# Kernel optimization log

Hardware: AMD Instinct MI355X
Metric: run time of the kernel (lower is better)

Reference implementation:

```python
import jax, jax.numpy as jnp
import numpy as np

DIM = 512
MOVE_EMBED_DIM = 64
NUM_BUCKETS = 64
EMBED = 768
B = 8192
STEPS = 10


def setup_inputs() -> dict:
    key = jax.random.key(0)
    ks = jax.random.split(key, 16)
    def g(i, shape, scale=0.02):
        return jax.random.normal(ks[i], shape, jnp.float32) * scale
    return {
        "boards": jax.random.normal(ks[0], (STEPS, B, EMBED), jnp.float32),
        "flags": jax.random.randint(ks[1], (STEPS - 2, B), 0, 2).astype(bool),
        "themes": jax.random.randint(ks[2], (B,), 0, 10),
        "moves": jax.random.randint(ks[3], (B,), 0, NUM_BUCKETS),
        "start": jax.random.uniform(ks[4], (DIM,), jnp.float32),
        "red_w": g(5, (DIM, EMBED)), "red_b": jnp.zeros((DIM,), jnp.float32),
        "ca_w": g(6, (DIM, DIM)), "ca_b": jnp.zeros((DIM,), jnp.float32),
        "cb_w": g(7, (DIM, DIM)), "cb_b": jnp.zeros((DIM,), jnp.float32),
        "move_emb": g(8, (NUM_BUCKETS, MOVE_EMBED_DIM), 1.0),
        "fc1_w": g(9, (DIM, DIM + MOVE_EMBED_DIM)), "fc1_b": jnp.zeros((DIM,), jnp.float32),
        "fc2_w": g(10, (DIM, DIM)), "fc2_b": jnp.zeros((DIM,), jnp.float32),
        "fc3_w": g(11, (1024, DIM)), "fc3_b": jnp.zeros((1024,), jnp.float32),
        "fc4_w": g(12, (1024, 1024)), "fc4_b": jnp.zeros((1024,), jnp.float32),
        "fc5_w": g(13, (512, 1024)), "fc5_b": jnp.zeros((512,), jnp.float32),
        "out_w": g(14, (1, 512)), "out_b": jnp.zeros((1,), jnp.float32),
    }


def reference(boards, flags, themes, moves, start, red_w, red_b, ca_w, ca_b,
              cb_w, cb_b, move_emb, fc1_w, fc1_b, fc2_w, fc2_b, fc3_w, fc3_b,
              fc4_w, fc4_b, fc5_w, fc5_b, out_w, out_b):
    bsz = boards.shape[1]
    # boards[0:2] are never masked; boards[2:10] are zeroed where flags are False
    full_flags = jnp.concatenate([jnp.ones((2, bsz), bool), flags], axis=0)  # [10,B]
    emb = jnp.where(full_flags[:, :, None], boards, 0.0)                     # [10,B,E]
    # shared dim reducer + relu applied to all 10 positions at once
    e = jax.nn.relu(jnp.einsum('sbe,de->sbd', emb, red_w) + red_b)           # [10,B,DIM]
    # precompute combiner_b contribution for every step (batched GEMM)
    eb = jnp.einsum('sbd,kd->sbk', e, cb_w) + cb_b                           # [10,B,DIM]
    # combiner_a(start)+combiner_b(e0) == combiner_a(h0)+... with h0 = start broadcast
    h0 = jnp.broadcast_to(start, (bsz, DIM))
    def step(h, eb_t):
        return jnp.tanh(h @ ca_w.T + ca_b + eb_t), None
    h, _ = jax.lax.scan(step, h0, eb)                                        # [B,DIM]
    # dropout layers are identity in eval mode
    m = move_emb[moves]                                                      # [B,MOVE_EMBED_DIM]
    x = jax.nn.relu(jnp.concatenate([h, m], axis=-1) @ fc1_w.T + fc1_b)
    x = jax.nn.relu(x @ fc2_w.T + fc2_b)
    x = jax.nn.relu(x @ fc3_w.T + fc3_b)
    x = jax.nn.relu(x @ fc4_w.T + fc4_b)
    x = jax.nn.relu(x @ fc5_w.T + fc5_b)
    return x @ out_w.T + out_b                                               # [B,1]
```

## Files before the change

### kernel.cpp

```cpp
#include <hip/hip_runtime.h>
#include <math.h>

#define BATCH  8192
#define EMBED  768
#define DIMD   512
#define MEDIM  64
#define NSTEP  10

typedef __bf16 bf16x8 __attribute__((ext_vector_type(8)));
typedef float  f32x4  __attribute__((ext_vector_type(4)));

__device__ __forceinline__ void load16_lds(const void* g, void* l)
{
    auto* gp = (__attribute__((address_space(1))) char*)(uintptr_t)g;
    auto* lp = (__attribute__((address_space(3))) char*)(unsigned int)(uintptr_t)l;
    __builtin_amdgcn_global_load_lds(gp, lp, 16, 0, 0);
}

#define BN 128
#define BK 32

template<int ACT, bool ADDEB, bool GATHER, int BMT>
__global__ __launch_bounds__(256)
void gemm_bf16(const __bf16* __restrict__ A, const __bf16* __restrict__ Bt,
               const float* __restrict__ bias, const __bf16* __restrict__ add,
               const __bf16* __restrict__ me, const int* __restrict__ moves,
               __bf16* __restrict__ C, int M, int N, int K)
{
    constexpr int NG = (BMT + BN) / 16;
    constexpr int AG = BMT / 16;
    constexpr int MR = BMT / 32;

    __shared__ __bf16 lds[(BMT + BN) * BK];

    const int nwg  = gridDim.x * gridDim.y;
    const int orig = blockIdx.y * gridDim.x + blockIdx.x;
    const int cpx  = nwg >> 3;
    const int swz  = (orig & 7) * cpx + (orig >> 3);
    const int bx   = swz % gridDim.x;
    const int by   = swz / gridDim.x;

    const int tid  = threadIdx.x;
    const int wave = tid >> 6;
    const int lane = tid & 63;
    const int row0 = by * BMT;
    const int col0 = bx * BN;

    const int wr = (wave >> 1) * (BMT / 2);
    const int wc = (wave & 1) * 64;
    const int fr = lane & 15;
    const int fk = (lane >> 4) * 8;

    const int srow = lane >> 2;
    const int skk  = (lane & 3) * 8;

    f32x4 acc[MR][4] = {};

    for (int k0 = 0; k0 < K; k0 += BK) {
#pragma unroll
        for (int ci = 0; ci < NG / 4; ++ci) {
            const int c = ci * 4 + wave;
            const int r = c * 16 + srow;
            const __bf16* g;
            if (c < AG) {
                if (GATHER) {
                    const int grow = row0 + r;
                    g = (k0 < DIMD)
                        ? (A  + (size_t)grow * DIMD + k0 + skk)
                        : (me + (size_t)moves[grow] * MEDIM + (k0 - DIMD) + skk);
                } else {
                    g = A + (size_t)(row0 + r) * K + k0 + skk;
                }
            } else {
                g = Bt + (size_t)(col0 + (r - BMT)) * K + k0 + skk;
            }
            load16_lds(g, &lds[c * 512]);
        }
        __syncthreads();

        const __bf16* As = lds;
        const __bf16* Bs = lds + BMT * BK;
        bf16x8 af[MR], bfr[4];
#pragma unroll
        for (int m = 0; m < MR; ++m)
            af[m] = *(const bf16x8*)&As[(wr + m * 16 + fr) * BK + fk];
#pragma unroll
        for (int n = 0; n < 4; ++n)
            bfr[n] = *(const bf16x8*)&Bs[(wc + n * 16 + fr) * BK + fk];
#pragma unroll
        for (int m = 0; m < MR; ++m)
#pragma unroll
            for (int n = 0; n < 4; ++n)
                acc[m][n] = __builtin_amdgcn_mfma_f32_16x16x32_bf16(
                                af[m], bfr[n], acc[m][n], 0, 0, 0);
        __syncthreads();
    }

#pragma unroll
    for (int m = 0; m < MR; ++m) {
#pragma unroll
        for (int n = 0; n < 4; ++n) {
            const int cc = col0 + wc + n * 16 + fr;
            const float bb = bias[cc];
#pragma unroll
            for (int j = 0; j < 4; ++j) {
                const int rr = row0 + wr + m * 16 + (lane >> 4) * 4 + j;
                float v = acc[m][n][j] + bb;
                if (ADDEB) v += (float)add[(size_t)rr * N + cc];
                if (ACT == 1) v = fmaxf(v, 0.0f);
                if (ACT == 2) {
                    const float p = __expf(2.0f * v);
                    v = 1.0f - 2.0f / (p + 1.0f);
                }
                C[(size_t)rr * N + cc] = (__bf16)v;
            }
        }
    }
}

__global__ __launch_bounds__(256)
void gemm_red_f32A(const float* __restrict__ A, const __bf16* __restrict__ Bt,
                   const float* __restrict__ bias, const int* __restrict__ flags,
                   __bf16* __restrict__ C, int M, int N, int K)
{
    __shared__ float  Af[128 * 32];
    __shared__ __bf16 Bs[128 * 32];

    const int nwg  = gridDim.x * gridDim.y;
    const int orig = blockIdx.y * gridDim.x + blockIdx.x;
    const int cpx  = nwg >> 3;
    const int swz  = (orig & 7) * cpx + (orig >> 3);
    const int bx   = swz % gridDim.x;
    const int by   = swz / gridDim.x;

    const int tid  = threadIdx.x;
    const int wave = tid >> 6;
    const int lane = tid & 63;
    const int row0 = by * 128;
    const int col0 = bx * BN;

    const int wr = (wave >> 1) * 64;
    const int wc = (wave & 1) * 64;
    const int fr = lane & 15;
    const int fk = (lane >> 4) * 8;

    const int asrow = lane >> 3;
    const int akc   = (lane & 7) ^ asrow;
    const int bsrow = lane >> 2;
    const int bskk  = (lane & 3) * 8;

    f32x4 acc[4][4] = {};

    for (int k0 = 0; k0 < K; k0 += BK) {
#pragma unroll
        for (int ci = 0; ci < 6; ++ci) {
            const int c = ci * 4 + wave;
            if (c < 16) {
                const float* g = A + (size_t)(row0 + c * 8 + asrow) * K + k0 + akc * 4;
                load16_lds(g, (char*)Af + c * 1024);
            } else {
                const int cb = c - 16;
                const __bf16* g = Bt + (size_t)(col0 + cb * 16 + bsrow) * K + k0 + bskk;
                load16_lds(g, (char*)Bs + cb * 1024);
            }
        }
        __syncthreads();

        bf16x8 af[4], bfr[4];
#pragma unroll
        for (int m = 0; m < 4; ++m) {
            const int r = wr + m * 16 + fr;
            const int kc0 = fk >> 2;
            const f32x4 v0 = *(const f32x4*)&Af[r * 32 + ((kc0    ) ^ (r & 7)) * 4];
            const f32x4 v1 = *(const f32x4*)&Af[r * 32 + ((kc0 + 1) ^ (r & 7)) * 4];
#pragma unroll
            for (int j = 0; j < 4; ++j) {
                af[m][j]     = (__bf16)v0[j];
                af[m][j + 4] = (__bf16)v1[j];
            }
        }
#pragma unroll
        for (int n = 0; n < 4; ++n)
            bfr[n] = *(const bf16x8*)&Bs[(wc + n * 16 + fr) * BK + fk];
#pragma unroll
        for (int m = 0; m < 4; ++m)
#pragma unroll
            for (int n = 0; n < 4; ++n)
                acc[m][n] = __builtin_amdgcn_mfma_f32_16x16x32_bf16(
                                af[m], bfr[n], acc[m][n], 0, 0, 0);
        __syncthreads();
    }

    float fl[4][4];
#pragma unroll
    for (int m = 0; m < 4; ++m)
#pragma unroll
        for (int j = 0; j < 4; ++j) {
            const int rr = row0 + wr + m * 16 + (lane >> 4) * 4 + j;
            const int s = rr >> 13, b = rr & 8191;
            fl[m][j] = (s < 2) ? 1.0f
                               : (flags[(size_t)(s - 2) * BATCH + b] ? 1.0f : 0.0f);
        }

#pragma unroll
    for (int m = 0; m < 4; ++m) {
#pragma unroll
        for (int n = 0; n < 4; ++n) {
            const int cc = col0 + wc + n * 16 + fr;
            const float bb = bias[cc];
#pragma unroll
            for (int j = 0; j < 4; ++j) {
                const int rr = row0 + wr + m * 16 + (lane >> 4) * 4 + j;
                const float a = (fl[m][j] != 0.0f) ? (acc[m][n][j] + bb) : bb;
                C[(size_t)rr * N + cc] = (__bf16)fmaxf(a, 0.0f);
            }
        }
    }
}

enum : int { W_RED = 0, W_CA = 393216, W_CB = 655360, W_FC1 = 917504,
             W_FC2 = 1212416, W_FC3 = 1474560, W_FC4 = 1998848,
             W_FC5 = 3047424, W_ME = 3571712, W_TOTAL = 3575808 };

__global__ __launch_bounds__(256)
void cvt_weights(const float* __restrict__ w0, const float* __restrict__ w1,
                 const float* __restrict__ w2, const float* __restrict__ w3,
                 const float* __restrict__ w4, const float* __restrict__ w5,
                 const float* __restrict__ w6, const float* __restrict__ w7,
                 const float* __restrict__ w8, __bf16* __restrict__ dst)
{
    const int idx = blockIdx.x * 256 + threadIdx.x;
    if (idx >= W_TOTAL / 8) return;
    const int e = idx * 8;
    const float* src; int off;
    if      (e < W_CA)  { src = w0; off = W_RED; }
    else if (e < W_CB)  { src = w1; off = W_CA; }
    else if (e < W_FC1) { src = w2; off = W_CB; }
    else if (e < W_FC2) { src = w3; off = W_FC1; }
    else if (e < W_FC3) { src = w4; off = W_FC2; }
    else if (e < W_FC4) { src = w5; off = W_FC3; }
    else if (e < W_FC5) { src = w6; off = W_FC4; }
    else if (e < W_ME)  { src = w7; off = W_FC5; }
    else                { src = w8; off = W_ME; }
    const float4 v0 = ((const float4*)(src + (e - off)))[0];
    const float4 v1 = ((const float4*)(src + (e - off)))[1];
    bf16x8 o;
    o[0] = (__bf16)v0.x; o[1] = (__bf16)v0.y; o[2] = (__bf16)v0.z; o[3] = (__bf16)v0.w;
    o[4] = (__bf16)v1.x; o[5] = (__bf16)v1.y; o[6] = (__bf16)v1.z; o[7] = (__bf16)v1.w;
    *(bf16x8*)(dst + (size_t)e) = o;
}

__global__ __launch_bounds__(256)
void gemv_start(const float* __restrict__ caw, const float* __restrict__ cab,
                const float* __restrict__ start, float* __restrict__ tmp)
{
    __shared__ float s[DIMD];
    for (int i = threadIdx.x; i < DIMD; i += 256) s[i] = start[i];
    __syncthreads();
    const int n = blockIdx.x * 256 + threadIdx.x;
    const float4* w = (const float4*)(caw + (size_t)n * DIMD);
    float acc = 0.0f;
#pragma unroll 8
    for (int k = 0; k < DIMD / 4; ++k) {
        const float4 wv = w[k];
        acc += wv.x * s[k * 4] + wv.y * s[k * 4 + 1] +
               wv.z * s[k * 4 + 2] + wv.w * s[k * 4 + 3];
    }
    tmp[n] = acc + cab[n];
}

__global__ __launch_bounds__(256)
void h1_init(const float* __restrict__ tmp, const __bf16* __restrict__ eb0,
             __bf16* __restrict__ h)
{
    const int idx = blockIdx.x * 256 + threadIdx.x;
    const int c8 = idx & 63;
    const bf16x8 e = ((const bf16x8*)eb0)[idx];
    bf16x8 o;
#pragma unroll
    for (int j = 0; j < 8; ++j) {
        const float v = tmp[c8 * 8 + j] + (float)e[j];
        const float p = __expf(2.0f * v);
        o[j] = (__bf16)(1.0f - 2.0f / (p + 1.0f));
    }
    ((bf16x8*)h)[idx] = o;
}

__global__ __launch_bounds__(256)
void out_head(const __bf16* __restrict__ x, const float* __restrict__ out_w,
              const float* __restrict__ out_b, float* __restrict__ out)
{
    const int wid  = threadIdx.x >> 6;
    const int lane = threadIdx.x & 63;
    const int row  = blockIdx.x * 4 + wid;
    const bf16x8 xv = *(const bf16x8*)(x + (size_t)row * DIMD + lane * 8);
    const float4 w0 = ((const float4*)out_w)[lane * 2];
    const float4 w1 = ((const float4*)out_w)[lane * 2 + 1];
    float s = (float)xv[0] * w0.x + (float)xv[1] * w0.y + (float)xv[2] * w0.z +
              (float)xv[3] * w0.w + (float)xv[4] * w1.x + (float)xv[5] * w1.y +
              (float)xv[6] * w1.z + (float)xv[7] * w1.w;
#pragma unroll
    for (int off = 32; off; off >>= 1) s += __shfl_down(s, off, 64);
    if (lane == 0) out[row] = s + out_b[0];
}

extern "C" void kernel_launch(void* const* d_in, const int* in_sizes, int n_in,
                              void* d_out, int out_size, void* d_ws, size_t ws_size,
                              hipStream_t stream)
{
    const float* boards  = (const float*)d_in[0];
    const int*   flags   = (const int*)  d_in[1];
    const int*   moves   = (const int*)  d_in[3];
    const float* start   = (const float*)d_in[4];
    const float* red_w   = (const float*)d_in[5];
    const float* red_b   = (const float*)d_in[6];
    const float* ca_w    = (const float*)d_in[7];
    const float* ca_b    = (const float*)d_in[8];
    const float* cb_w    = (const float*)d_in[9];
    const float* cb_b    = (const float*)d_in[10];
    const float* move_emb= (const float*)d_in[11];
    const float* fc1_w   = (const float*)d_in[12];
    const float* fc1_b   = (const float*)d_in[13];
    const float* fc2_w   = (const float*)d_in[14];
    const float* fc2_b   = (const float*)d_in[15];
    const float* fc3_w   = (const float*)d_in[16];
    const float* fc3_b   = (const float*)d_in[17];
    const float* fc4_w   = (const float*)d_in[18];
    const float* fc4_b   = (const float*)d_in[19];
    const float* fc5_w   = (const float*)d_in[20];
    const float* fc5_b   = (const float*)d_in[21];
    const float* out_w   = (const float*)d_in[22];
    const float* out_b   = (const float*)d_in[23];

    __bf16* wsb = (__bf16*)d_ws;
    __bf16* wpool  = wsb;
    __bf16* e_all  = wsb + 3575808;
    __bf16* eb_all = wsb + 45518848;
    __bf16* hA     = wsb + 87461888;
    __bf16* hB     = wsb + 91656192;
    float*  tmpv   = (float*)(wsb + 95850496);
    __bf16* x1     = wsb + 96874496;
    __bf16* x2     = wsb + 101068800;
    __bf16* x3     = wsb + 105263104;
    __bf16* x4     = wsb + 113651712;
    __bf16* x5     = wsb + 122040320;

    const dim3 blk(256);

    cvt_weights<<<1746, blk, 0, stream>>>(red_w, ca_w, cb_w, fc1_w, fc2_w,
                                          fc3_w, fc4_w, fc5_w, move_emb, wpool);
    gemv_start<<<2, blk, 0, stream>>>(ca_w, ca_b, start, tmpv);

    gemm_red_f32A<<<dim3(4, 640), blk, 0, stream>>>(
        boards, wpool + W_RED, red_b, flags, e_all, NSTEP * BATCH, DIMD, EMBED);
    gemm_bf16<0, false, false, 128><<<dim3(4, 640), blk, 0, stream>>>(
        e_all, wpool + W_CB, cb_b, nullptr, nullptr, nullptr, eb_all,
        NSTEP * BATCH, DIMD, DIMD);

    h1_init<<<2048, blk, 0, stream>>>(tmpv, eb_all, hA);

    __bf16* hcur = hA;
    __bf16* hnxt = hB;
    for (int s = 1; s < NSTEP; ++s) {
        const __bf16* ebs = eb_all + (size_t)s * BATCH * DIMD;
        gemm_bf16<2, true, false, 64><<<dim3(4, 128), blk, 0, stream>>>(
            hcur, wpool + W_CA, ca_b, ebs, nullptr, nullptr, hnxt,
            BATCH, DIMD, DIMD);
        __bf16* t = hcur; hcur = hnxt; hnxt = t;
    }

    gemm_bf16<1, false, true, 128><<<dim3(4, 64), blk, 0, stream>>>(
        hcur, wpool + W_FC1, fc1_b, nullptr, wpool + W_ME, moves, x1,
        BATCH, DIMD, DIMD + MEDIM);
    gemm_bf16<1, false, false, 128><<<dim3(4, 64), blk, 0, stream>>>(
        x1, wpool + W_FC2, fc2_b, nullptr, nullptr, nullptr, x2, BATCH, DIMD, DIMD);
    gemm_bf16<1, false, false, 128><<<dim3(8, 64), blk, 0, stream>>>(
        x2, wpool + W_FC3, fc3_b, nullptr, nullptr, nullptr, x3, BATCH, 1024, DIMD);
    gemm_bf16<1, false, false, 128><<<dim3(8, 64), blk, 0, stream>>>(
        x3, wpool + W_FC4, fc4_b, nullptr, nullptr, nullptr, x4, BATCH, 1024, 1024);
    gemm_bf16<1, false, false, 128><<<dim3(4, 64), blk, 0, stream>>>(
        x4, wpool + W_FC5, fc5_b, nullptr, nullptr, nullptr, x5, BATCH, DIMD, 1024);

    out_head<<<BATCH / 4, blk, 0, stream>>>(x5, out_w, out_b, (float*)d_out);
}
```

Before: 491.8 us.

## Double-buffer LDS tiles in GEMM kernels to overlap loads with MFMA

Result: faster. 452.8 us (-7.9%).

```diff
diff --git a/kernel.cpp b/kernel.cpp
--- a/kernel.cpp
+++ b/kernel.cpp
@@ -31,7 +31,7 @@
     constexpr int AG = BMT / 16;
     constexpr int MR = BMT / 32;
 
-    __shared__ __bf16 lds[(BMT + BN) * BK];
+    __shared__ __bf16 lds[2][(BMT + BN) * BK];
 
     const int nwg  = gridDim.x * gridDim.y;
     const int orig = blockIdx.y * gridDim.x + blockIdx.x;
@@ -54,9 +54,7 @@
     const int srow = lane >> 2;
     const int skk  = (lane & 3) * 8;
 
-    f32x4 acc[MR][4] = {};
-
-    for (int k0 = 0; k0 < K; k0 += BK) {
+    auto stage = [&](int buf, int k0) {
 #pragma unroll
         for (int ci = 0; ci < NG / 4; ++ci) {
             const int c = ci * 4 + wave;
@@ -74,12 +72,22 @@
             } else {
                 g = Bt + (size_t)(col0 + (r - BMT)) * K + k0 + skk;
             }
-            load16_lds(g, &lds[c * 512]);
-        }
-        __syncthreads();
-
-        const __bf16* As = lds;
-        const __bf16* Bs = lds + BMT * BK;
+            load16_lds(g, &lds[buf][c * 512]);
+        }
+    };
+
+    f32x4 acc[MR][4] = {};
+
+    stage(0, 0);
+    __syncthreads();
+
+    const int NT = K / BK;
+    int cur = 0;
+    for (int t = 0; t < NT; ++t) {
+        if (t + 1 < NT) stage(cur ^ 1, (t + 1) * BK);
+
+        const __bf16* As = lds[cur];
+        const __bf16* Bs = lds[cur] + BMT * BK;
         bf16x8 af[MR], bfr[4];
 #pragma unroll
         for (int m = 0; m < MR; ++m)
@@ -94,6 +102,7 @@
                 acc[m][n] = __builtin_amdgcn_mfma_f32_16x16x32_bf16(
                                 af[m], bfr[n], acc[m][n], 0, 0, 0);
         __syncthreads();
+        cur ^= 1;
     }
 
 #pragma unroll
@@ -123,8 +132,8 @@
                    const float* __restrict__ bias, const int* __restrict__ flags,
                    __bf16* __restrict__ C, int M, int N, int K)
 {
-    __shared__ float  Af[128 * 32];
-    __shared__ __bf16 Bs[128 * 32];
+    __shared__ float  Af[2][128 * 32];
+    __shared__ __bf16 Bs[2][128 * 32];
 
     const int nwg  = gridDim.x * gridDim.y;
     const int orig = blockIdx.y * gridDim.x + blockIdx.x;
@@ -149,30 +158,38 @@
     const int bsrow = lane >> 2;
     const int bskk  = (lane & 3) * 8;
 
-    f32x4 acc[4][4] = {};
-
-    for (int k0 = 0; k0 < K; k0 += BK) {
+    auto stage = [&](int buf, int k0) {
 #pragma unroll
         for (int ci = 0; ci < 6; ++ci) {
             const int c = ci * 4 + wave;
             if (c < 16) {
                 const float* g = A + (size_t)(row0 + c * 8 + asrow) * K + k0 + akc * 4;
-                load16_lds(g, (char*)Af + c * 1024);
+                load16_lds(g, (char*)Af[buf] + c * 1024);
             } else {
                 const int cb = c - 16;
                 const __bf16* g = Bt + (size_t)(col0 + cb * 16 + bsrow) * K + k0 + bskk;
-                load16_lds(g, (char*)Bs + cb * 1024);
+                load16_lds(g, (char*)Bs[buf] + cb * 1024);
             }
         }
-        __syncthreads();
+    };
+
+    f32x4 acc[4][4] = {};
+
+    stage(0, 0);
+    __syncthreads();
+
+    const int NT = K / BK;
+    int cur = 0;
+    for (int t = 0; t < NT; ++t) {
+        if (t + 1 < NT) stage(cur ^ 1, (t + 1) * BK);
 
         bf16x8 af[4], bfr[4];
 #pragma unroll
         for (int m = 0; m < 4; ++m) {
             const int r = wr + m * 16 + fr;
             const int kc0 = fk >> 2;
-            const f32x4 v0 = *(const f32x4*)&Af[r * 32 + ((kc0    ) ^ (r & 7)) * 4];
-            const f32x4 v1 = *(const f32x4*)&Af[r * 32 + ((kc0 + 1) ^ (r & 7)) * 4];
+            const f32x4 v0 = *(const f32x4*)&Af[cur][r * 32 + ((kc0    ) ^ (r & 7)) * 4];
+            const f32x4 v1 = *(const f32x4*)&Af[cur][r * 32 + ((kc0 + 1) ^ (r & 7)) * 4];
 #pragma unroll
             for (int j = 0; j < 4; ++j) {
                 af[m][j]     = (__bf16)v0[j];
@@ -181,7 +198,7 @@
         }
 #pragma unroll
         for (int n = 0; n < 4; ++n)
-            bfr[n] = *(const bf16x8*)&Bs[(wc + n * 16 + fr) * BK + fk];
+            bfr[n] = *(const bf16x8*)&Bs[cur][(wc + n * 16 + fr) * BK + fk];
 #pragma unroll
         for (int m = 0; m < 4; ++m)
 #pragma unroll
@@ -189,6 +206,7 @@
                 acc[m][n] = __builtin_amdgcn_mfma_f32_16x16x32_bf16(
                                 af[m], bfr[n], acc[m][n], 0, 0, 0);
         __syncthreads();
+        cur ^= 1;
     }
 
     float fl[4][4];
```
